# Optimization experiments

Hardware: AMD Instinct MI355X
Metric: run time of the kernel (lower is better)

The kernel has to match this reference:

```python
import jax, jax.numpy as jnp
import numpy as np

DIM, HEADS, HD = 1536, 12, 128
B, F, H, W = 1, 8, 16, 28
L = F * H * W  # 3584
EPS = 1e-6


def setup_inputs() -> dict:
    key = jax.random.key(0)
    ks = jax.random.split(key, 8)
    s = 0.02
    x = jax.random.normal(ks[0], (B, L, DIM), jnp.float32)
    # RoPE tables: angles pos * theta_j, shape [1024, HD//2]
    ang = jnp.arange(1024, dtype=jnp.float32)[:, None] / (
        10000.0 ** (jnp.arange(HD // 2, dtype=jnp.float32) / (HD // 2)))
    freqs_cos = jnp.cos(ang)
    freqs_sin = jnp.sin(ang)
    Wq = jax.random.normal(ks[1], (DIM, DIM), jnp.float32) * s
    Wk = jax.random.normal(ks[2], (DIM, DIM), jnp.float32) * s
    Wv = jax.random.normal(ks[3], (DIM, DIM), jnp.float32) * s
    Wo = jax.random.normal(ks[4], (DIM, DIM), jnp.float32) * s
    zb = jnp.zeros((DIM,), jnp.float32)
    return dict(x=x, freqs_cos=freqs_cos, freqs_sin=freqs_sin,
                Wq=Wq, bq=zb, Wk=Wk, bk=zb, Wv=Wv, bv=zb, Wo=Wo, bo=zb,
                gq=jnp.ones((DIM,), jnp.float32), gk=jnp.ones((DIM,), jnp.float32),
                f=F, h=H, w=W)


def rms_norm(t, g, eps=EPS):
    # WanRMSNorm: x * rsqrt(mean(x^2) + eps) * weight, over last dim (full `dim`)
    return t * jax.lax.rsqrt(jnp.mean(t * t, axis=-1, keepdims=True) + eps) * g


def rope_apply(t, f, h, w, cos, sin):
    # t: [B, L, H, D]; 3D rope with per-axis frequency splits [c-2(c//3), c//3, c//3]
    B_, L_, H_, D_ = t.shape
    c = D_ // 2
    s0 = c - 2 * (c // 3)
    s1 = c // 3

    def build(tab):
        tf = jnp.broadcast_to(tab[:f, :s0][:, None, None, :], (f, h, w, s0))
        th = jnp.broadcast_to(tab[:h, s0:s0 + s1][None, :, None, :], (f, h, w, s1))
        tw = jnp.broadcast_to(tab[:w, s0 + s1:c][None, None, :, :], (f, h, w, s1))
        return jnp.concatenate([tf, th, tw], axis=-1).reshape(f * h * w, c)[:L_]

    cs = build(cos)[None, :, None, :]  # [1, L, 1, c]
    sn = build(sin)[None, :, None, :]
    tp = t.reshape(B_, L_, H_, c, 2)   # consecutive pairs -> complex (re, im)
    tr, ti = tp[..., 0], tp[..., 1]
    out_r = tr * cs - ti * sn
    out_i = tr * sn + ti * cs
    return jnp.stack([out_r, out_i], axis=-1).reshape(B_, L_, H_, D_)


def reference(x, freqs_cos, freqs_sin, Wq, bq, Wk, bk, Wv, bv, Wo, bo, gq, gk, f, h, w):
    B_, L_, _ = x.shape
    q = rms_norm(x @ Wq.T + bq, gq).reshape(B_, L_, HEADS, HD)
    k = rms_norm(x @ Wk.T + bk, gk).reshape(B_, L_, HEADS, HD)
    v = (x @ Wv.T + bv).reshape(B_, L_, HEADS, HD)
    q = rope_apply(q, f, h, w, freqs_cos, freqs_sin)
    k = rope_apply(k, f, h, w, freqs_cos, freqs_sin)
    scale = 1.0 / np.sqrt(HD).astype(np.float32)
    att = jax.nn.softmax(jnp.einsum('bqhd,bkhd->bhqk', q, k) * scale, axis=-1)
    o = jnp.einsum('bhqk,bkhd->bqhd', att, v).reshape(B_, L_, DIM)
    return o @ Wo.T + bo
```

## Files before the change

### kernel.cpp

```cpp
#include <hip/hip_runtime.h>
#include <hip/hip_bf16.h>


#define DIM   1536
#define HEADS 12
#define HD    128
#define LSEQ  3584

typedef __bf16 bf16_t;
typedef __attribute__((ext_vector_type(8))) __bf16 bf16x8;
typedef __attribute__((ext_vector_type(4))) float f32x4;
typedef __attribute__((ext_vector_type(16))) float f32x16;
typedef unsigned int u32;
typedef __attribute__((ext_vector_type(2))) unsigned int u32x2;
typedef __attribute__((ext_vector_type(4))) unsigned int u32x4;

static __device__ __forceinline__ ushort f2bf(float f) {
  bf16_t h = (bf16_t)f;
  return __builtin_bit_cast(ushort, h);
}
static __device__ __forceinline__ float bf2f(ushort u) {
  return (float)__builtin_bit_cast(bf16_t, u);
}
static __device__ __forceinline__ u32 pkbf(float a, float b) {
  return (u32)f2bf(a) | ((u32)f2bf(b) << 16);
}

static __device__ __forceinline__ void plswap(u32& x, u32& y, int hi) {
#if __has_builtin(__builtin_amdgcn_permlane32_swap)
  (void)hi;
  u32x2 r = __builtin_amdgcn_permlane32_swap(x, y, false, false);
  x = r[0]; y = r[1];
#else
  u32 sx = __shfl_xor(x, 32, 64);
  u32 sy = __shfl_xor(y, 32, 64);
  u32 nx = hi ? sy : x;
  u32 ny = hi ? y : sx;
  x = nx; y = ny;
#endif
}

__global__ __launch_bounds__(256) void cvt_f32_bf16(const float* __restrict__ in,
                                                    ushort* __restrict__ out, int n) {
  int i = (blockIdx.x * 256 + threadIdx.x) * 4;
  if (i + 3 < n) {
    float4 v = *reinterpret_cast<const float4*>(in + i);
    ushort4 o;
    o.x = f2bf(v.x); o.y = f2bf(v.y); o.z = f2bf(v.z); o.w = f2bf(v.w);
    *reinterpret_cast<ushort4*>(out + i) = o;
  }
}

template <int SEGS, bool OUT_F32>
__global__ __launch_bounds__(256) void gemm_bt(const ushort* __restrict__ A,
                                               const ushort* __restrict__ B,
                                               const float* __restrict__ bias0,
                                               const float* __restrict__ bias1,
                                               const float* __restrict__ bias2,
                                               void* __restrict__ Cout) {
  const int K = DIM;
  __shared__ __attribute__((aligned(16))) ushort As[128 * 32];
  __shared__ __attribute__((aligned(16))) ushort Bs[128 * 32];
  const int tid  = threadIdx.x;
  const int lane = tid & 63;
  const int wid  = tid >> 6;
  const int m0 = blockIdx.x * 128;
  const int n0 = blockIdx.y * 128;
  const int wm = (wid >> 1) * 64;
  const int wn = (wid & 1) * 64;
  const int lr = lane & 15;
  const int lg = lane >> 4;
  const int crow = lane >> 2;
  const int ccol = (lane & 3) * 8;

  f32x4 acc[4][4] = {};

  for (int kt = 0; kt < K; kt += 32) {
    __syncthreads();
#pragma unroll
    for (int i = 0; i < 2; ++i) {
      int chunk = wid * 2 + i;
      int row = chunk * 16 + crow;
      const ushort* ga = A + (size_t)(m0 + row) * K + kt + ccol;
      const ushort* gb = B + (size_t)(n0 + row) * K + kt + ccol;
      __builtin_amdgcn_global_load_lds(
          (__attribute__((address_space(1))) void*)(void*)ga,
          (__attribute__((address_space(3))) void*)(&As[chunk * 512]), 16, 0, 0);
      __builtin_amdgcn_global_load_lds(
          (__attribute__((address_space(1))) void*)(void*)gb,
          (__attribute__((address_space(3))) void*)(&Bs[chunk * 512]), 16, 0, 0);
    }
    __syncthreads();

    bf16x8 af[4], bfr[4];
#pragma unroll
    for (int m = 0; m < 4; ++m)
      af[m] = *reinterpret_cast<const bf16x8*>(&As[(wm + m * 16 + lr) * 32 + lg * 8]);
#pragma unroll
    for (int n = 0; n < 4; ++n)
      bfr[n] = *reinterpret_cast<const bf16x8*>(&Bs[(wn + n * 16 + lr) * 32 + lg * 8]);
#pragma unroll
    for (int m = 0; m < 4; ++m)
#pragma unroll
      for (int n = 0; n < 4; ++n)
        acc[m][n] = __builtin_amdgcn_mfma_f32_16x16x32_bf16(af[m], bfr[n], acc[m][n], 0, 0, 0);
  }

  int seg = 0;
  const float* bp = bias0;
  if (SEGS == 3) {
    seg = n0 >= 2 * DIM ? 2 : (n0 >= DIM ? 1 : 0);
    bp = seg == 0 ? bias0 : (seg == 1 ? bias1 : bias2);
  }
  const int nbase = n0 - seg * DIM;

#pragma unroll
  for (int m = 0; m < 4; ++m) {
#pragma unroll
    for (int n = 0; n < 4; ++n) {
      int col = nbase + wn + n * 16 + lr;
      float bvv = bp[col];
#pragma unroll
      for (int r = 0; r < 4; ++r) {
        int row = m0 + wm + m * 16 + lg * 4 + r;
        float v = acc[m][n][r] + bvv;
        if (OUT_F32)
          ((float*)Cout)[(size_t)row * DIM + col] = v;
        else
          ((ushort*)Cout)[(size_t)seg * ((size_t)LSEQ * DIM) + (size_t)row * DIM + col] = f2bf(v);
      }
    }
  }
}

__global__ __launch_bounds__(256) void normrope(ushort* __restrict__ Qb,
                                                ushort* __restrict__ Kb,
                                                const float* __restrict__ gq,
                                                const float* __restrict__ gk,
                                                const float* __restrict__ cosT,
                                                const float* __restrict__ sinT) {
  __shared__ float red[4];
  const int l = blockIdx.x;
  const int tid = threadIdx.x;
  ushort* row = (blockIdx.y == 0 ? Qb : Kb) + (size_t)l * DIM;
  const float* g = blockIdx.y == 0 ? gq : gk;

  const u32* rp = reinterpret_cast<const u32*>(row);
  u32 pk[3];
  float v[6];
#pragma unroll
  for (int i = 0; i < 3; ++i) {
    pk[i] = rp[tid * 3 + i];
    v[2 * i]     = bf2f((ushort)(pk[i] & 0xffff));
    v[2 * i + 1] = bf2f((ushort)(pk[i] >> 16));
  }
  float ss = 0.f;
#pragma unroll
  for (int i = 0; i < 6; ++i) ss += v[i] * v[i];
#pragma unroll
  for (int off = 1; off < 64; off <<= 1) ss += __shfl_xor(ss, off, 64);
  if ((tid & 63) == 0) red[tid >> 6] = ss;
  __syncthreads();
  float tot = red[0] + red[1] + red[2] + red[3];
  float rms = rsqrtf(tot * (1.0f / DIM) + 1e-6f);

  const int fi = l / 448;
  const int rem = l % 448;
  const int hi = rem / 28;
  const int wi = rem % 28;

  u32* wp = reinterpret_cast<u32*>(row);
#pragma unroll
  for (int i = 0; i < 3; ++i) {
    int p = tid * 3 + i;
    int head = p >> 6;
    int j = p & 63;
    int trow = (j < 22) ? fi : ((j < 43) ? hi : wi);
    float cv = cosT[trow * 64 + j];
    float sv = sinT[trow * 64 + j];
    int idx = head * 128 + 2 * j;
    float xr = v[2 * i] * rms * g[idx];
    float xi = v[2 * i + 1] * rms * g[idx + 1];
    float orr = xr * cv - xi * sv;
    float oii = xr * sv + xi * cv;
    wp[p] = (u32)f2bf(orr) | ((u32)f2bf(oii) << 16);
  }
}

#define QBLK 128
#define KVB  64

__global__ __launch_bounds__(256, 2) void attn(const ushort* __restrict__ Q,
                                               const ushort* __restrict__ Kp,
                                               const ushort* __restrict__ Vp,
                                               ushort* __restrict__ O,
                                               float* __restrict__ Opart,
                                               float* __restrict__ mlbuf) {
  __shared__ __attribute__((aligned(16))) ushort Ks[KVB * 128];
  __shared__ __attribute__((aligned(16))) ushort Vt[128][72];
  const int tid  = threadIdx.x;
  const int lane = tid & 63;
  const int wv   = tid >> 6;
  const int lq   = lane & 31;
  const int hi   = lane >> 5;
  const int h    = blockIdx.y;
  const int q0   = blockIdx.x * QBLK;
  const float scale = 0.08838834764831845f;

  const int split  = blockIdx.z;
  const int nsplit = gridDim.z;
  const int NT     = LSEQ / KVB;
  const int t_lo   = split * NT / nsplit;
  const int t_hi   = (split + 1) * NT / nsplit;

  bf16x8 qf[8];
  {
    const ushort* qbase = Q + (size_t)(q0 + wv * 32 + lq) * DIM + h * HD;
#pragma unroll
    for (int d = 0; d < 8; ++d)
      qf[d] = *reinterpret_cast<const bf16x8*>(qbase + d * 16 + hi * 8);
  }

  f32x16 accO[4] = {};
  float m = -1e30f, lsum = 0.f;

  const int mbk = tid >> 4;
  const int mbd = tid & 15;

  for (int t = t_lo; t < t_hi; ++t) {
    const int kv0 = t * KVB;
    __syncthreads();
#pragma unroll
    for (int i = 0; i < 4; ++i) {
      int o16 = (wv * 4 + i) * 64 + lane;
      int r = o16 >> 4;
      int b = (o16 & 15) * 16;
      int srcu = (b ^ ((r & 7) << 4)) >> 1;
      const ushort* gp = Kp + (size_t)(kv0 + r) * DIM + h * HD + srcu;
      __builtin_amdgcn_global_load_lds(
          (__attribute__((address_space(1))) void*)(void*)gp,
          (__attribute__((address_space(3))) void*)(&Ks[(wv * 4 + i) * 512]), 16, 0, 0);
    }
    {
      const ushort* vbase = Vp + (size_t)(kv0 + mbk * 4) * DIM + h * HD + mbd * 8;
      uint4 r0 = *reinterpret_cast<const uint4*>(vbase);
      uint4 r1 = *reinterpret_cast<const uint4*>(vbase + DIM);
      uint4 r2 = *reinterpret_cast<const uint4*>(vbase + 2 * DIM);
      uint4 r3 = *reinterpret_cast<const uint4*>(vbase + 3 * DIM);
      const ushort* s0 = reinterpret_cast<const ushort*>(&r0);
      const ushort* s1 = reinterpret_cast<const ushort*>(&r1);
      const ushort* s2 = reinterpret_cast<const ushort*>(&r2);
      const ushort* s3 = reinterpret_cast<const ushort*>(&r3);
#pragma unroll
      for (int jj = 0; jj < 8; ++jj) {
        int j = (jj + mbd) & 7;
        uint2 w;
        w.x = (u32)s0[j] | ((u32)s1[j] << 16);
        w.y = (u32)s2[j] | ((u32)s3[j] << 16);
        *reinterpret_cast<uint2*>(&Vt[mbd * 8 + j][mbk * 4]) = w;
      }
    }
    __syncthreads();

#pragma unroll
    for (int hf = 0; hf < 2; ++hf) {
      f32x16 sv = {};
#pragma unroll
      for (int d = 0; d < 8; ++d) {
        int db = d * 32 + hi * 16;
        const bf16x8 a = *reinterpret_cast<const bf16x8*>(
            (const char*)Ks + (hf * 32 + lq) * 256 + (db ^ ((lq & 7) << 4)));
        sv = __builtin_amdgcn_mfma_f32_32x32x16_bf16(a, qf[d], sv, 0, 0, 0);
      }

      float pmax = sv[0];
#pragma unroll
      for (int r = 1; r < 16; ++r) pmax = fmaxf(pmax, sv[r]);
      pmax = fmaxf(pmax, __shfl_xor(pmax, 32, 64));
      pmax *= scale;

      if (__any(pmax > m + 8.f)) {
        float mn = fmaxf(m, pmax);
        float al = __expf(m - mn);
        m = mn;
        lsum *= al;
#pragma unroll
        for (int r = 0; r < 16; ++r) {
          int qr = (r & 3) + 8 * (r >> 2) + 4 * hi;
          float alr = __shfl(al, qr, 64);
          accO[0][r] *= alr; accO[1][r] *= alr;
          accO[2][r] *= alr; accO[3][r] *= alr;
        }
      }

      float p[16];
      float psum = 0.f;
#pragma unroll
      for (int r = 0; r < 16; ++r) {
        p[r] = __expf(fmaf(sv[r], scale, -m));
        psum += p[r];
      }
      psum += __shfl_xor(psum, 32, 64);
      lsum += psum;

      u32 a0 = pkbf(p[0], p[1]),   a1 = pkbf(p[2], p[3]);
      u32 a4 = pkbf(p[4], p[5]),   a5 = pkbf(p[6], p[7]);
      u32 c0 = pkbf(p[8], p[9]),   c1 = pkbf(p[10], p[11]);
      u32 c4 = pkbf(p[12], p[13]), c5 = pkbf(p[14], p[15]);
      plswap(a0, a4, hi);
      plswap(a1, a5, hi);
      plswap(c0, c4, hi);
      plswap(c1, c5, hi);
      u32x4 w0 = {a0, a1, a4, a5};
      u32x4 w1 = {c0, c1, c4, c5};
      bf16x8 pa0 = __builtin_bit_cast(bf16x8, w0);
      bf16x8 pa1 = __builtin_bit_cast(bf16x8, w1);

#pragma unroll
      for (int nd = 0; nd < 4; ++nd) {
        bf16x8 vb0 = *reinterpret_cast<const bf16x8*>(
            &Vt[nd * 32 + lq][hf * 32 + hi * 8]);
        accO[nd] = __builtin_amdgcn_mfma_f32_32x32x16_bf16(pa0, vb0, accO[nd], 0, 0, 0);
      }
#pragma unroll
      for (int nd = 0; nd < 4; ++nd) {
        bf16x8 vb1 = *reinterpret_cast<const bf16x8*>(
            &Vt[nd * 32 + lq][hf * 32 + 16 + hi * 8]);
        accO[nd] = __builtin_amdgcn_mfma_f32_32x32x16_bf16(pa1, vb1, accO[nd], 0, 0, 0);
      }
    }
  }

  if (gridDim.z == 1) {
    float inv_own = 1.0f / lsum;
#pragma unroll
    for (int r = 0; r < 16; ++r) {
      int qr = (r & 3) + 8 * (r >> 2) + 4 * hi;
      float inv = __shfl(inv_own, qr, 64);
      ushort* orow = O + (size_t)(q0 + wv * 32 + qr) * DIM + h * HD;
#pragma unroll
      for (int nd = 0; nd < 4; ++nd)
        orow[nd * 32 + lq] = f2bf(accO[nd][r] * inv);
    }
  } else {
    float* Op = Opart + ((size_t)split * HEADS + h) * ((size_t)LSEQ * HD);
#pragma unroll
    for (int r = 0; r < 16; ++r) {
      int qr = (r & 3) + 8 * (r >> 2) + 4 * hi;
      float* orow = Op + (size_t)(q0 + wv * 32 + qr) * HD;
#pragma unroll
      for (int nd = 0; nd < 4; ++nd)
        orow[nd * 32 + lq] = accO[nd][r];
    }
    if (hi == 0) {
      size_t row = (size_t)split * (HEADS * LSEQ) + (size_t)h * LSEQ + (q0 + wv * 32 + lq);
      mlbuf[2 * row]     = m;
      mlbuf[2 * row + 1] = lsum;
    }
  }
}

__global__ __launch_bounds__(256) void attn_merge(const float* __restrict__ Opart,
                                                  const float* __restrict__ mlbuf,
                                                  ushort* __restrict__ Ob, int nsplit) {
  const int RN = HEADS * LSEQ;
  int gi = blockIdx.x * 256 + threadIdx.x;
  int row = gi >> 5;
  int d4 = (gi & 31) * 4;
  if (row >= RN) return;
  int h = row / LSEQ, q = row % LSEQ;

  float M = -1e30f;
  for (int s = 0; s < nsplit; ++s) M = fmaxf(M, mlbuf[2 * ((size_t)s * RN + row)]);
  float den = 0.f;
  float4 acc = {0.f, 0.f, 0.f, 0.f};
  for (int s = 0; s < nsplit; ++s) {
    float ms = mlbuf[2 * ((size_t)s * RN + row)];
    float ls = mlbuf[2 * ((size_t)s * RN + row) + 1];
    float w = __expf(ms - M);
    den += ls * w;
    const float4 o = *reinterpret_cast<const float4*>(
        &Opart[((size_t)s * RN + row) * HD + d4]);
    acc.x += w * o.x; acc.y += w * o.y; acc.z += w * o.z; acc.w += w * o.w;
  }
  float inv = 1.0f / den;
  ushort4 r;
  r.x = f2bf(acc.x * inv); r.y = f2bf(acc.y * inv);
  r.z = f2bf(acc.z * inv); r.w = f2bf(acc.w * inv);
  *reinterpret_cast<ushort4*>(&Ob[(size_t)q * DIM + h * HD + d4]) = r;
}

extern "C" void kernel_launch(void* const* d_in, const int* in_sizes, int n_in,
                              void* d_out, int out_size, void* d_ws, size_t ws_size,
                              hipStream_t stream) {
  (void)in_sizes; (void)n_in; (void)out_size;
  const float* x    = (const float*)d_in[0];
  const float* cosT = (const float*)d_in[1];
  const float* sinT = (const float*)d_in[2];
  const float* Wq   = (const float*)d_in[3];
  const float* bq   = (const float*)d_in[4];
  const float* Wk   = (const float*)d_in[5];
  const float* bk   = (const float*)d_in[6];
  const float* Wv   = (const float*)d_in[7];
  const float* bv_in = (const float*)d_in[8];
  const float* Wo   = (const float*)d_in[9];
  const float* bo   = (const float*)d_in[10];
  const float* gq   = (const float*)d_in[11];
  const float* gk   = (const float*)d_in[12];

  const size_t LD = (size_t)LSEQ * DIM;
  const size_t WD = (size_t)DIM * DIM;
  const size_t base_bytes = (5 * LD + 4 * WD) * sizeof(ushort);
  if (ws_size < base_bytes) return;

  ushort* xb  = (ushort*)d_ws;
  ushort* Wqb = xb + LD;
  ushort* Wkb = Wqb + WD;
  ushort* Wvb = Wkb + WD;
  ushort* Wob = Wvb + WD;
  ushort* Qb  = Wob + WD;
  ushort* Kb  = Qb + LD;
  ushort* Vb  = Kb + LD;
  ushort* Ob  = Vb + LD;

  const size_t RN = (size_t)HEADS * LSEQ;
  const size_t split_bytes = RN * HD * 4 + RN * 8;
  int nsplit = 1;
  if (ws_size >= base_bytes + 3 * split_bytes) nsplit = 3;
  else if (ws_size >= base_bytes + 2 * split_bytes) nsplit = 2;
  float* Opart = (float*)((char*)d_ws + base_bytes);
  float* mlbuf = Opart + (size_t)nsplit * RN * HD;

  cvt_f32_bf16<<<(int)(LD / 4 / 256), 256, 0, stream>>>(x, xb, (int)LD);
  cvt_f32_bf16<<<(int)(WD / 4 / 256), 256, 0, stream>>>(Wq, Wqb, (int)WD);
  cvt_f32_bf16<<<(int)(WD / 4 / 256), 256, 0, stream>>>(Wk, Wkb, (int)WD);
  cvt_f32_bf16<<<(int)(WD / 4 / 256), 256, 0, stream>>>(Wv, Wvb, (int)WD);
  cvt_f32_bf16<<<(int)(WD / 4 / 256), 256, 0, stream>>>(Wo, Wob, (int)WD);

  gemm_bt<3, false><<<dim3(LSEQ / 128, 3 * DIM / 128), 256, 0, stream>>>(
      xb, Wqb, bq, bk, bv_in, Qb);

  normrope<<<dim3(LSEQ, 2), 256, 0, stream>>>(Qb, Kb, gq, gk, cosT, sinT);

  attn<<<dim3(LSEQ / QBLK, HEADS, nsplit), 256, 0, stream>>>(Qb, Kb, Vb, Ob, Opart, mlbuf);
  if (nsplit > 1)
    attn_merge<<<(int)(RN * 32 / 256), 256, 0, stream>>>(Opart, mlbuf, Ob, nsplit);

  gemm_bt<1, true><<<dim3(LSEQ / 128, DIM / 128), 256, 0, stream>>>(
      Ob, Wob, bo, bo, bo, d_out);
}
```

Before: 322.4 us.

## Double-buffer K/V tiles in attention and raise wave priority around MFMA

The attention kernel now keeps two LDS buffers for K and the transposed V. The next tile's K (via global_load_lds) and V (into registers) are issued before computing on the current tile, so global latency overlaps with MFMA work. It also wraps the MFMA sections with s_setprio. The cost is double the LDS footprint and extra live V registers, which may reduce occupancy under launch_bounds(256,2).

```diff
diff --git a/kernel.cpp b/kernel.cpp
--- a/kernel.cpp
+++ b/kernel.cpp
@@ -196,8 +196,8 @@
                                                ushort* __restrict__ O,
                                                float* __restrict__ Opart,
                                                float* __restrict__ mlbuf) {
-  __shared__ __attribute__((aligned(16))) ushort Ks[KVB * 128];
-  __shared__ __attribute__((aligned(16))) ushort Vt[128][72];
+  __shared__ __attribute__((aligned(16))) ushort Ks[2][KVB * 128];
+  __shared__ __attribute__((aligned(16))) ushort Vt[2][128][72];
   const int tid  = threadIdx.x;
   const int lane = tid & 63;
   const int wv   = tid >> 6;
@@ -227,9 +227,9 @@
   const int mbk = tid >> 4;
   const int mbd = tid & 15;
 
-  for (int t = t_lo; t < t_hi; ++t) {
+  uint4 vr0, vr1, vr2, vr3;
+  auto issueK = [&](int t, int nb) {
     const int kv0 = t * KVB;
-    __syncthreads();
 #pragma unroll
     for (int i = 0; i < 4; ++i) {
       int o16 = (wv * 4 + i) * 64 + lane;
@@ -239,39 +239,56 @@
       const ushort* gp = Kp + (size_t)(kv0 + r) * DIM + h * HD + srcu;
       __builtin_amdgcn_global_load_lds(
           (__attribute__((address_space(1))) void*)(void*)gp,
-          (__attribute__((address_space(3))) void*)(&Ks[(wv * 4 + i) * 512]), 16, 0, 0);
-    }
-    {
-      const ushort* vbase = Vp + (size_t)(kv0 + mbk * 4) * DIM + h * HD + mbd * 8;
-      uint4 r0 = *reinterpret_cast<const uint4*>(vbase);
-      uint4 r1 = *reinterpret_cast<const uint4*>(vbase + DIM);
-      uint4 r2 = *reinterpret_cast<const uint4*>(vbase + 2 * DIM);
-      uint4 r3 = *reinterpret_cast<const uint4*>(vbase + 3 * DIM);
-      const ushort* s0 = reinterpret_cast<const ushort*>(&r0);
-      const ushort* s1 = reinterpret_cast<const ushort*>(&r1);
-      const ushort* s2 = reinterpret_cast<const ushort*>(&r2);
-      const ushort* s3 = reinterpret_cast<const ushort*>(&r3);
-#pragma unroll
-      for (int jj = 0; jj < 8; ++jj) {
-        int j = (jj + mbd) & 7;
-        uint2 w;
-        w.x = (u32)s0[j] | ((u32)s1[j] << 16);
-        w.y = (u32)s2[j] | ((u32)s3[j] << 16);
-        *reinterpret_cast<uint2*>(&Vt[mbd * 8 + j][mbk * 4]) = w;
-      }
-    }
+          (__attribute__((address_space(3))) void*)(&Ks[nb][(wv * 4 + i) * 512]), 16, 0, 0);
+    }
+  };
+  auto loadV = [&](int t) {
+    const ushort* vbase = Vp + (size_t)(t * KVB + mbk * 4) * DIM + h * HD + mbd * 8;
+    vr0 = *reinterpret_cast<const uint4*>(vbase);
+    vr1 = *reinterpret_cast<const uint4*>(vbase + DIM);
+    vr2 = *reinterpret_cast<const uint4*>(vbase + 2 * DIM);
+    vr3 = *reinterpret_cast<const uint4*>(vbase + 3 * DIM);
+  };
+  auto writeV = [&](int nb) {
+    const ushort* s0 = reinterpret_cast<const ushort*>(&vr0);
+    const ushort* s1 = reinterpret_cast<const ushort*>(&vr1);
+    const ushort* s2 = reinterpret_cast<const ushort*>(&vr2);
+    const ushort* s3 = reinterpret_cast<const ushort*>(&vr3);
+#pragma unroll
+    for (int jj = 0; jj < 8; ++jj) {
+      int j = (jj + mbd) & 7;
+      uint2 w;
+      w.x = (u32)s0[j] | ((u32)s1[j] << 16);
+      w.y = (u32)s2[j] | ((u32)s3[j] << 16);
+      *reinterpret_cast<uint2*>(&Vt[nb][mbd * 8 + j][mbk * 4]) = w;
+    }
+  };
+
+  issueK(t_lo, 0);
+  loadV(t_lo);
+
+  int buf = 0;
+  for (int t = t_lo; t < t_hi; ++t) {
+    writeV(buf);
     __syncthreads();
+
+    if (t + 1 < t_hi) {
+      issueK(t + 1, buf ^ 1);
+      loadV(t + 1);
+    }
 
 #pragma unroll
     for (int hf = 0; hf < 2; ++hf) {
       f32x16 sv = {};
+      __builtin_amdgcn_s_setprio(1);
 #pragma unroll
       for (int d = 0; d < 8; ++d) {
         int db = d * 32 + hi * 16;
         const bf16x8 a = *reinterpret_cast<const bf16x8*>(
-            (const char*)Ks + (hf * 32 + lq) * 256 + (db ^ ((lq & 7) << 4)));
+            (const char*)&Ks[buf][0] + (hf * 32 + lq) * 256 + (db ^ ((lq & 7) << 4)));
         sv = __builtin_amdgcn_mfma_f32_32x32x16_bf16(a, qf[d], sv, 0, 0, 0);
       }
+      __builtin_amdgcn_s_setprio(0);
 
       float pmax = sv[0];
 #pragma unroll
@@ -316,19 +333,24 @@
       bf16x8 pa0 = __builtin_bit_cast(bf16x8, w0);
       bf16x8 pa1 = __builtin_bit_cast(bf16x8, w1);
 
+      __builtin_amdgcn_s_setprio(1);
 #pragma unroll
       for (int nd = 0; nd < 4; ++nd) {
         bf16x8 vb0 = *reinterpret_cast<const bf16x8*>(
-            &Vt[nd * 32 + lq][hf * 32 + hi * 8]);
+            &Vt[buf][nd * 32 + lq][hf * 32 + hi * 8]);
         accO[nd] = __builtin_amdgcn_mfma_f32_32x32x16_bf16(pa0, vb0, accO[nd], 0, 0, 0);
       }
 #pragma unroll
       for (int nd = 0; nd < 4; ++nd) {
         bf16x8 vb1 = *reinterpret_cast<const bf16x8*>(
-            &Vt[nd * 32 + lq][hf * 32 + 16 + hi * 8]);
+            &Vt[buf][nd * 32 + lq][hf * 32 + 16 + hi * 8]);
         accO[nd] = __builtin_amdgcn_mfma_f32_32x32x16_bf16(pa1, vb1, accO[nd], 0, 0, 0);
       }
-    }
+      __builtin_amdgcn_s_setprio(0);
+    }
+
+    __syncthreads();
+    buf ^= 1;
   }
 
   if (gridDim.z == 1) {
```

After: 303.1 us. 6.0% less time.
